# Performance work log

Measured on AMD Instinct MI355X. Metric: run time of the kernel, lower is better.

Reference implementation:

```python
import jax, jax.numpy as jnp
import numpy as np

NUM_HEADS = 8
LN_EPS = 1e-5  # torch.nn.LayerNorm default


def setup_inputs() -> dict:
    key = jax.random.key(0)
    k1, k2, k3, k4 = jax.random.split(key, 4)
    B, S, H = 32, 512, 256
    inputs = jax.random.normal(k1, (B, S, H), dtype=jnp.float32)
    radial_mask = jax.random.uniform(k2, (B, S), dtype=jnp.float32, minval=1e-4, maxval=1.0)
    # torch Linear stores weight as [out, in]; init ~ U(-1/sqrt(in), 1/sqrt(in))
    bound = 1.0 / np.sqrt(H)
    in_proj_w = jax.random.uniform(k3, (3 * H, H), dtype=jnp.float32, minval=-bound, maxval=bound)
    out_proj_w = jax.random.uniform(k4, (H, H), dtype=jnp.float32, minval=-bound, maxval=bound)
    ln_gamma = jnp.ones((H,), dtype=jnp.float32)
    ln_beta = jnp.zeros((H,), dtype=jnp.float32)
    return {
        "inputs": inputs,
        "radial_mask": radial_mask,
        "in_proj_w": in_proj_w,
        "out_proj_w": out_proj_w,
        "ln_gamma": ln_gamma,
        "ln_beta": ln_beta,
    }


def reference(inputs, radial_mask, in_proj_w, out_proj_w, ln_gamma, ln_beta):
    B, S, H = inputs.shape
    nh = NUM_HEADS
    hd = H // nh

    # LayerNorm over the last dim
    mu = jnp.mean(inputs, axis=-1, keepdims=True)
    var = jnp.var(inputs, axis=-1, keepdims=True)
    normed = (inputs - mu) * jax.lax.rsqrt(var + LN_EPS) * ln_gamma + ln_beta

    # QKV projection (no bias); torch Linear: x @ W.T
    qkv = jnp.einsum('bsh,oh->bso', normed, in_proj_w)
    q, k, v = jnp.split(qkv, 3, axis=-1)

    # [B, S, H] -> [B, nh, S, hd]
    def to_heads(x):
        return x.reshape(B, S, nh, hd).transpose(0, 2, 1, 3)

    q = to_heads(q)
    k = to_heads(k)
    v = to_heads(v)

    # Custom transforms before SDPA
    q = q * q + 1e-6
    k = k + jnp.log(radial_mask)[:, None, :, None]

    # scaled_dot_product_attention with default scale = 1/sqrt(hd)
    scale = 1.0 / np.sqrt(hd).astype(np.float32)
    scores = jnp.einsum('bhqd,bhkd->bhqk', q, k) * scale
    attn = jax.nn.softmax(scores, axis=-1)
    out = jnp.einsum('bhqk,bhkd->bhqd', attn, v)

    # back to [B, S, H], output projection, residual with 1/sqrt(2)
    out = out.transpose(0, 2, 1, 3).reshape(B, S, H)
    out = jnp.einsum('bsh,oh->bso', out, out_proj_w)
    return (out + inputs) * np.float32(0.5 ** 0.5)
```

## Files before the change

kernel.cpp:

```cpp
#include <hip/hip_runtime.h>
#include <hip/hip_bf16.h>

typedef unsigned int u32;
typedef unsigned short u16;

#define B_   32
#define S_   512
#define H_   256
#define NH_  8
#define HD_  32

typedef __attribute__((ext_vector_type(8))) short short8;
typedef __attribute__((ext_vector_type(4))) float f32x4;

__device__ __forceinline__ float bfl(u32 u){ union{u32 i;float f;} c; c.i = u << 16;          return c.f; }
__device__ __forceinline__ float bfh(u32 u){ union{u32 i;float f;} c; c.i = u & 0xffff0000u;  return c.f; }
__device__ __forceinline__ float bf1(u16 u){ union{u32 i;float f;} c; c.i = ((u32)u) << 16;   return c.f; }
__device__ __forceinline__ u16   f2b(float f){ __hip_bfloat16 h = __float2bfloat16(f); return *reinterpret_cast<u16*>(&h); }
__device__ __forceinline__ u32   pk2(float a, float b){ return (u32)f2b(a) | ((u32)f2b(b) << 16); }
__device__ __forceinline__ void  unp8(const uint4 u, float* f){
  f[0]=bfl(u.x); f[1]=bfh(u.x); f[2]=bfl(u.y); f[3]=bfh(u.y);
  f[4]=bfl(u.z); f[5]=bfh(u.z); f[6]=bfl(u.w); f[7]=bfh(u.w);
}
__device__ __forceinline__ f32x4 mfma16(short8 a, short8 b, f32x4 c){
  return __builtin_amdgcn_mfma_f32_16x16x32_bf16(a, b, c, 0, 0, 0);
}

template<int F32>
__device__ __forceinline__ void load8(const void* p, int e8, float* f) {
  if (F32) {
    const float4* q = (const float4*)p;
    const float4 a = q[e8 * 2], b = q[e8 * 2 + 1];
    f[0]=a.x; f[1]=a.y; f[2]=a.z; f[3]=a.w; f[4]=b.x; f[5]=b.y; f[6]=b.z; f[7]=b.w;
  } else {
    unp8(((const uint4*)p)[e8], f);
  }
}
template<int F32>
__device__ __forceinline__ void store8(void* p, int e8, const float* f) {
  if (F32) {
    float4* q = (float4*)p;
    q[e8 * 2]     = make_float4(f[0], f[1], f[2], f[3]);
    q[e8 * 2 + 1] = make_float4(f[4], f[5], f[6], f[7]);
  } else {
    uint4 u;
    u.x = pk2(f[0], f[1]); u.y = pk2(f[2], f[3]);
    u.z = pk2(f[4], f[5]); u.w = pk2(f[6], f[7]);
    ((uint4*)p)[e8] = u;
  }
}
template<int F32>
__device__ __forceinline__ float load1(const void* p, size_t e) {
  return F32 ? ((const float*)p)[e] : bf1(((const u16*)p)[e]);
}
template<int F32>
__device__ __forceinline__ short8 loadBfrag(const void* wp, int row, int k0, int K) {
  if (F32) {
    const float* w = (const float*)wp + (size_t)row * K + k0;
    const float4 a = *(const float4*)w;
    const float4 b = *(const float4*)(w + 4);
    short8 r;
    r[0]=(short)f2b(a.x); r[1]=(short)f2b(a.y); r[2]=(short)f2b(a.z); r[3]=(short)f2b(a.w);
    r[4]=(short)f2b(b.x); r[5]=(short)f2b(b.y); r[6]=(short)f2b(b.z); r[7]=(short)f2b(b.w);
    return r;
  } else {
    return *(const short8*)((const u16*)wp + (size_t)row * K + k0);
  }
}

__device__ __forceinline__ int sniff_mode(const void* xin) {
  __shared__ int votes;
  const int tid = threadIdx.x;
  if (tid == 0) votes = 0;
  __syncthreads();
  const u32* xw = (const u32*)xin;
  int h = 0;
#pragma unroll
  for (int j = 0; j < 4; ++j) {
    const u32 u = xw[(tid << 2) + j];
    const u32 e = (u >> 7) & 0xFF;
    h += (e >= 100 && e <= 135) ? 1 : 0;
  }
  if (h) atomicAdd(&votes, h);
  __syncthreads();
  return (votes >= 512) ? 0 : 1;
}

template<int F32>
__global__ __launch_bounds__(256) void ln_qkv_mfma(
    const void* __restrict__ xin, const void* __restrict__ rmask,
    const void* __restrict__ wi, const void* __restrict__ gamma,
    const void* __restrict__ beta,
    u16* __restrict__ qbuf, u16* __restrict__ kbuf, u16* __restrict__ vt)
{
  if (sniff_mode(xin) != F32) return;

  __shared__ __align__(16) u16 XnF[2 * 8 * 64 * 8];
  __shared__ __align__(16) u16 TR[4][32 * 20];
  __shared__ float lmr[32];
  const int tid = threadIdx.x;
  const int l = tid & 63, w = tid >> 6;
  const int lr = l & 15, quad = l >> 4;
  const int row0 = (blockIdx.x >> 1) * 32;
  const int nhalf = blockIdx.x & 1;

  {
    const int r = tid >> 5, ln = tid & 31;
    float g[8], bb[8];
    load8<F32>(gamma, ln, g);
    load8<F32>(beta,  ln, bb);
    const int c = ln >> 2, qd = ln & 3;
#pragma unroll
    for (int p = 0; p < 4; ++p) {
      const int R = p * 8 + r;
      const int grow = row0 + R;
      float x[8]; load8<F32>(xin, grow * 32 + ln, x);
      float s = 0.f, sq = 0.f;
#pragma unroll
      for (int j = 0; j < 8; ++j) { s += x[j]; sq += x[j] * x[j]; }
#pragma unroll
      for (int m = 1; m < 32; m <<= 1) { s += __shfl_xor(s, m); sq += __shfl_xor(sq, m); }
      const float mu  = s * (1.f / 256.f);
      const float var = sq * (1.f / 256.f) - mu * mu;
      const float rs  = rsqrtf(var + 1e-5f);
      short8 pk;
#pragma unroll
      for (int j = 0; j < 8; ++j) pk[j] = (short)f2b((x[j] - mu) * rs * g[j] + bb[j]);
      const int t = R >> 4, rm = R & 15;
      *(short8*)(XnF + (((t * 8 + c) * 64 + qd * 16 + rm) << 3)) = pk;
      if (ln == 0) lmr[R] = logf(load1<F32>(rmask, grow));
    }
  }
  __syncthreads();

  const int bb_ = row0 >> 9;
  const int sB  = (row0 & 511);
  const int tbase = nhalf * 24 + w * 6;
  u16* trw = TR[w];

  short8 BfA[8], BfB[8];
#pragma unroll
  for (int c = 0; c < 8; ++c)
    BfA[c] = loadBfrag<F32>(wi, tbase * 16 + lr, c * 32 + quad * 8, 256);

#pragma unroll
  for (int nt = 0; nt < 6; ++nt) {
    short8* cur = (nt & 1) ? BfB : BfA;
    short8* nxt = (nt & 1) ? BfA : BfB;
    if (nt < 5) {
#pragma unroll
      for (int c = 0; c < 8; ++c)
        nxt[c] = loadBfrag<F32>(wi, (tbase + nt + 1) * 16 + lr, c * 32 + quad * 8, 256);
    }

    f32x4 a0 = {0.f,0.f,0.f,0.f}, a1 = {0.f,0.f,0.f,0.f};
#pragma unroll
    for (int c = 0; c < 8; ++c) {
      const short8 f0 = *(const short8*)(XnF + ((c       * 64 + l) << 3));
      const short8 f1 = *(const short8*)(XnF + (((8 + c) * 64 + l) << 3));
      a0 = mfma16(f0, cur[c], a0);
      a1 = mfma16(f1, cur[c], a1);
    }

    const int nAbs  = (tbase + nt) * 16;
    const int type  = nAbs >> 8;
    const int dbase = nAbs & 255;
    const int bh    = bb_ * NH_ + (dbase >> 5);
    if (type < 2) {
#pragma unroll
      for (int m = 0; m < 2; ++m) {
        const f32x4 acc = m ? a1 : a0;
        const int sL = m * 16 + quad * 4;
#pragma unroll
        for (int i = 0; i < 4; ++i) {
          float v = acc[i];
          v = (type == 0) ? (v * v + 1e-6f) : (v + lmr[sL + i]);
          trw[(sL + i) * 20 + lr] = f2b(v);
        }
      }
      const int s = l >> 1, half = l & 1;
      const uint2 lo = *(const uint2*)(trw + s * 20 + half * 8);
      const uint2 hi = *(const uint2*)(trw + s * 20 + half * 8 + 4);
      uint4 ov; ov.x = lo.x; ov.y = lo.y; ov.z = hi.x; ov.w = hi.y;
      u16* dst = (type == 0) ? qbuf : kbuf;
      *(uint4*)(dst + ((size_t)bh * S_ + sB + s) * HD_ + (dbase & 31) + half * 8) = ov;
    } else {
      const int dd = (dbase & 255) + lr;
#pragma unroll
      for (int m = 0; m < 2; ++m) {
        const f32x4 acc = m ? a1 : a0;
        const int dv = (dbase - 512 + lr) & 255;
        const int hv = dv >> 5, ddv = dv & 31;
        const int bhv = bb_ * NH_ + hv;
        const int slot16 = (((sB >> 5) * 2 + (ddv >> 4)) * 4 + quad) * 16 + (ddv & 15);
        uint2 pkv;
        pkv.x = pk2(acc[0], acc[1]);
        pkv.y = pk2(acc[2], acc[3]);
        *(uint2*)(vt + (size_t)bhv * (S_ * HD_) + slot16 * 8 + m * 4) = pkv;
      }
      (void)dd;
    }
  }
}

__global__ __launch_bounds__(256, 4) void attn_mfma(
    const u16* __restrict__ qbuf, const u16* __restrict__ kbuf,
    const u16* __restrict__ vt, u16* __restrict__ ctx)
{
  __shared__ __align__(16) u16 OB[4][16 * 40];
  const int tid = threadIdx.x;
  const int bh = blockIdx.x & 255, sq = blockIdx.x >> 8;
  const int l = tid & 63, w = tid >> 6;
  const int lr = l & 15, quad = l >> 4;
  const size_t kvbase = (size_t)bh * (S_ * HD_);
  const int q0 = sq * 64 + w * 16;

  const float cE = 0.17677669529663688f * 1.4426950408889634f;

  const short8 qf = *(const short8*)(qbuf + kvbase + (size_t)(q0 + lr) * HD_ + quad * 8);
  const u16* kp = kbuf + kvbase + (size_t)lr * HD_ + quad * 8;
  const u16* vp = vt + kvbase;

  float mS = -1e30f, lS = 0.f;
  f32x4 o0 = {0.f,0.f,0.f,0.f}, o1 = {0.f,0.f,0.f,0.f};

#pragma unroll
  for (int c = 0; c < 4; ++c) {
    f32x4 acc[8];
#pragma unroll
    for (int j = 0; j < 8; ++j) {
      const short8 kf = *(const short8*)(kp + (c * 8 + j) * (16 * HD_));
      f32x4 z = {0.f,0.f,0.f,0.f};
      acc[j] = mfma16(kf, qf, z);
    }

    float mc = acc[0][0];
#pragma unroll
    for (int j = 0; j < 8; ++j)
#pragma unroll
      for (int r = 0; r < 4; ++r) mc = fmaxf(mc, acc[j][r]);
    mc = fmaxf(mc, __shfl_xor(mc, 16));
    mc = fmaxf(mc, __shfl_xor(mc, 32));
    const float mNew  = fmaxf(mS, mc * cE);
    const float alpha = exp2f(mS - mNew);
    float sc = 0.f;
#pragma unroll
    for (int j = 0; j < 8; ++j)
#pragma unroll
      for (int r = 0; r < 4; ++r) {
        const float p = exp2f(fmaf(acc[j][r], cE, -mNew));
        acc[j][r] = p; sc += p;
      }
    sc += __shfl_xor(sc, 16);
    sc += __shfl_xor(sc, 32);
    lS = fmaf(lS, alpha, sc);
    mS = mNew;
#pragma unroll
    for (int r = 0; r < 4; ++r) { o0[r] *= alpha; o1[r] *= alpha; }

#pragma unroll
    for (int g = 0; g < 4; ++g) {
      union { u32 u[4]; short8 s; } pa;
      pa.u[0] = pk2(acc[2*g][0],   acc[2*g][1]);
      pa.u[1] = pk2(acc[2*g][2],   acc[2*g][3]);
      pa.u[2] = pk2(acc[2*g+1][0], acc[2*g+1][1]);
      pa.u[3] = pk2(acc[2*g+1][2], acc[2*g+1][3]);
      const int c16 = c * 4 + g;
      const short8 v0 = *(const short8*)(vp + (((c16 * 8 +     quad) * 16 + lr) << 3));
      const short8 v1 = *(const short8*)(vp + (((c16 * 8 + 4 + quad) * 16 + lr) << 3));
      o0 = mfma16(pa.s, v0, o0);
      o1 = mfma16(pa.s, v1, o1);
    }
  }
  const float inv = 1.f / lS;

  u16* ob = OB[w];
#pragma unroll
  for (int r = 0; r < 4; ++r) {
    const int qq = quad * 4 + r;
    const float iv = __shfl(inv, (l & 48) | qq);
    ob[qq * 40 + lr]      = f2b(o0[r] * iv);
    ob[qq * 40 + 16 + lr] = f2b(o1[r] * iv);
  }
  const uint4 ov = *(const uint4*)(ob + (l >> 2) * 40 + (l & 3) * 8);
  *(uint4*)(ctx + kvbase + (size_t)(q0 + (l >> 2)) * HD_ + (l & 3) * 8) = ov;
}

template<int F32>
__global__ __launch_bounds__(256) void proj_mfma(
    const u16* __restrict__ ctx, const void* __restrict__ xin,
    const void* __restrict__ wo, void* __restrict__ out)
{
  if (sniff_mode(xin) != F32) return;

  __shared__ __align__(16) u16 XnF[8 * 64 * 8];
  __shared__ __align__(16) u16 OutB[16 * 264];
  const int tid = threadIdx.x;
  const int l = tid & 63, w = tid >> 6;
  const int lr = l & 15, quad = l >> 4;
  const int row0 = blockIdx.x * 16;
  const int b = row0 >> 9, s0 = row0 & 511;

#pragma unroll
  for (int it = 0; it < 2; ++it) {
    const int idx = it * 256 + tid;
    const int dq = idx & 3, sl = (idx >> 2) & 15, h = idx >> 6;
    const uint4 cv = *(const uint4*)(ctx + ((size_t)(b * 8 + h) * S_ + s0 + sl) * HD_ + dq * 8);
    const int qds = dq ^ (sl & 3);
    *(uint4*)(XnF + ((h * 64 + qds * 16 + sl) << 3)) = cv;
  }
  __syncthreads();

  const int lsw = (quad ^ (lr & 3)) * 16 + lr;
  short8 BfA[8], BfB[8];
#pragma unroll
  for (int c = 0; c < 8; ++c)
    BfA[c] = loadBfrag<F32>(wo, (w * 4) * 16 + lr, c * 32 + quad * 8, 256);

#pragma unroll
  for (int nt = 0; nt < 4; ++nt) {
    short8* cur = (nt & 1) ? BfB : BfA;
    short8* nxt = (nt & 1) ? BfA : BfB;
    if (nt < 3) {
#pragma unroll
      for (int c = 0; c < 8; ++c)
        nxt[c] = loadBfrag<F32>(wo, (w * 4 + nt + 1) * 16 + lr, c * 32 + quad * 8, 256);
    }
    const int n0 = (w * 4 + nt) * 16;
    f32x4 a0 = {0.f,0.f,0.f,0.f};
#pragma unroll
    for (int c = 0; c < 8; ++c) {
      const short8 f0 = *(const short8*)(XnF + ((c * 64 + lsw) << 3));
      a0 = mfma16(f0, cur[c], a0);
    }
#pragma unroll
    for (int i = 0; i < 4; ++i)
      OutB[(quad * 4 + i) * 264 + n0 + lr] = f2b(a0[i]);
  }
  __syncthreads();

  const int r  = tid >> 4;
  const int c8 = (tid & 15) * 2;
#pragma unroll
  for (int j8 = 0; j8 < 2; ++j8) {
    float xv[8]; load8<F32>(xin, (row0 + r) * 32 + c8 + j8, xv);
    float pv[8]; unp8(*(const uint4*)(OutB + r * 264 + (c8 + j8) * 8), pv);
    float ov[8];
#pragma unroll
    for (int j = 0; j < 8; ++j) ov[j] = (pv[j] + xv[j]) * 0.70710678f;
    store8<F32>(out, (row0 + r) * 32 + c8 + j8, ov);
  }
}

extern "C" void kernel_launch(void* const* d_in, const int* in_sizes, int n_in,
                              void* d_out, int out_size, void* d_ws, size_t ws_size,
                              hipStream_t stream)
{
  const void* xin   = d_in[0];
  const void* rmask = d_in[1];
  const void* wi    = d_in[2];
  const void* wo    = d_in[3];
  const void* gam   = d_in[4];
  const void* bet   = d_in[5];

  u16* q   = (u16*)d_ws;
  u16* k   = q + 4194304;
  u16* vt  = k + 4194304;
  u16* cxb = vt + 4194304;

  ln_qkv_mfma<0><<<1024, 256, 0, stream>>>(xin, rmask, wi, gam, bet, q, k, vt);
  ln_qkv_mfma<1><<<1024, 256, 0, stream>>>(xin, rmask, wi, gam, bet, q, k, vt);
  attn_mfma     <<<2048, 256, 0, stream>>>(q, k, vt, cxb);
  proj_mfma<0>  <<<1024, 256, 0, stream>>>(cxb, xin, wo, d_out);
  proj_mfma<1>  <<<1024, 256, 0, stream>>>(cxb, xin, wo, d_out);
}
```

Before: 204.6 us.

## Enlarge QKV row tile to 64, keep A fragments in registers, direct stores

The LN+QKV kernel now handles 64 rows per block instead of 32, so each weight B-fragment load feeds four MFMA row tiles instead of two. The grid is halved and launch bounds are set to two blocks per CU. The normalized A fragments are hoisted into registers once, and the LDS transpose staging for Q/K is dropped in favour of direct scalar bf16 stores to global. The output projection also hoists its A fragments from LDS, and the dtype-sniff vote now uses a wave ballot instead of per-thread atomics. The trade-off is much higher register pressure and uncoalesced 2-byte Q/K global stores, and the tighter 2-block launch bound may cause spills.

```diff
diff --git a/kernel.cpp b/kernel.cpp
--- a/kernel.cpp
+++ b/kernel.cpp
@@ -81,13 +81,14 @@
     const u32 e = (u >> 7) & 0xFF;
     h += (e >= 100 && e <= 135) ? 1 : 0;
   }
-  if (h) atomicAdd(&votes, h);
-  __syncthreads();
-  return (votes >= 512) ? 0 : 1;
-}
-
-template<int F32>
-__global__ __launch_bounds__(256) void ln_qkv_mfma(
+  const unsigned long long m = __ballot(h >= 3);
+  if ((tid & 63) == 0) atomicAdd(&votes, __popcll(m));
+  __syncthreads();
+  return (votes >= 128) ? 0 : 1;
+}
+
+template<int F32>
+__global__ __launch_bounds__(256, 2) void ln_qkv_mfma(
     const void* __restrict__ xin, const void* __restrict__ rmask,
     const void* __restrict__ wi, const void* __restrict__ gamma,
     const void* __restrict__ beta,
@@ -95,13 +96,12 @@
 {
   if (sniff_mode(xin) != F32) return;
 
-  __shared__ __align__(16) u16 XnF[2 * 8 * 64 * 8];
-  __shared__ __align__(16) u16 TR[4][32 * 20];
-  __shared__ float lmr[32];
+  __shared__ __align__(16) u16 XnF[4 * 8 * 64 * 8];
+  __shared__ float lmr[64];
   const int tid = threadIdx.x;
   const int l = tid & 63, w = tid >> 6;
   const int lr = l & 15, quad = l >> 4;
-  const int row0 = (blockIdx.x >> 1) * 32;
+  const int row0 = (blockIdx.x >> 1) * 64;
   const int nhalf = blockIdx.x & 1;
 
   {
@@ -111,7 +111,7 @@
     load8<F32>(beta,  ln, bb);
     const int c = ln >> 2, qd = ln & 3;
 #pragma unroll
-    for (int p = 0; p < 4; ++p) {
+    for (int p = 0; p < 8; ++p) {
       const int R = p * 8 + r;
       const int grow = row0 + R;
       float x[8]; load8<F32>(xin, grow * 32 + ln, x);
@@ -133,72 +133,72 @@
   }
   __syncthreads();
 
+  short8 Af[4][8];
+#pragma unroll
+  for (int mt = 0; mt < 4; ++mt)
+#pragma unroll
+    for (int c = 0; c < 8; ++c)
+      Af[mt][c] = *(const short8*)(XnF + (((mt * 8 + c) * 64 + l) << 3));
+
   const int bb_ = row0 >> 9;
-  const int sB  = (row0 & 511);
+  const int sB  = row0 & 511;
   const int tbase = nhalf * 24 + w * 6;
-  u16* trw = TR[w];
-
-  short8 BfA[8], BfB[8];
+
+  short8 Bf[2][8];
 #pragma unroll
   for (int c = 0; c < 8; ++c)
-    BfA[c] = loadBfrag<F32>(wi, tbase * 16 + lr, c * 32 + quad * 8, 256);
+    Bf[0][c] = loadBfrag<F32>(wi, tbase * 16 + lr, c * 32 + quad * 8, 256);
 
 #pragma unroll
   for (int nt = 0; nt < 6; ++nt) {
-    short8* cur = (nt & 1) ? BfB : BfA;
-    short8* nxt = (nt & 1) ? BfA : BfB;
+    const int cb = nt & 1;
     if (nt < 5) {
 #pragma unroll
       for (int c = 0; c < 8; ++c)
-        nxt[c] = loadBfrag<F32>(wi, (tbase + nt + 1) * 16 + lr, c * 32 + quad * 8, 256);
-    }
-
-    f32x4 a0 = {0.f,0.f,0.f,0.f}, a1 = {0.f,0.f,0.f,0.f};
+        Bf[cb ^ 1][c] = loadBfrag<F32>(wi, (tbase + nt + 1) * 16 + lr, c * 32 + quad * 8, 256);
+    }
+
+    f32x4 a[4];
+#pragma unroll
+    for (int mt = 0; mt < 4; ++mt) a[mt] = (f32x4){0.f, 0.f, 0.f, 0.f};
 #pragma unroll
     for (int c = 0; c < 8; ++c) {
-      const short8 f0 = *(const short8*)(XnF + ((c       * 64 + l) << 3));
-      const short8 f1 = *(const short8*)(XnF + (((8 + c) * 64 + l) << 3));
-      a0 = mfma16(f0, cur[c], a0);
-      a1 = mfma16(f1, cur[c], a1);
+#pragma unroll
+      for (int mt = 0; mt < 4; ++mt)
+        a[mt] = mfma16(Af[mt][c], Bf[cb][c], a[mt]);
     }
 
     const int nAbs  = (tbase + nt) * 16;
     const int type  = nAbs >> 8;
     const int dbase = nAbs & 255;
-    const int bh    = bb_ * NH_ + (dbase >> 5);
     if (type < 2) {
-#pragma unroll
-      for (int m = 0; m < 2; ++m) {
-        const f32x4 acc = m ? a1 : a0;
-        const int sL = m * 16 + quad * 4;
+      const int d  = dbase + lr;
+      const int h  = d >> 5, dd = d & 31;
+      const int bh = bb_ * NH_ + h;
+      u16* dst = (type == 0) ? qbuf : kbuf;
+#pragma unroll
+      for (int mt = 0; mt < 4; ++mt) {
+        const int sL = mt * 16 + quad * 4;
 #pragma unroll
         for (int i = 0; i < 4; ++i) {
-          float v = acc[i];
+          float v = a[mt][i];
           v = (type == 0) ? (v * v + 1e-6f) : (v + lmr[sL + i]);
-          trw[(sL + i) * 20 + lr] = f2b(v);
+          dst[((size_t)bh * S_ + sB + sL + i) * HD_ + dd] = f2b(v);
         }
       }
-      const int s = l >> 1, half = l & 1;
-      const uint2 lo = *(const uint2*)(trw + s * 20 + half * 8);
-      const uint2 hi = *(const uint2*)(trw + s * 20 + half * 8 + 4);
-      uint4 ov; ov.x = lo.x; ov.y = lo.y; ov.z = hi.x; ov.w = hi.y;
-      u16* dst = (type == 0) ? qbuf : kbuf;
-      *(uint4*)(dst + ((size_t)bh * S_ + sB + s) * HD_ + (dbase & 31) + half * 8) = ov;
     } else {
-      const int dd = (dbase & 255) + lr;
-#pragma unroll
-      for (int m = 0; m < 2; ++m) {
-        const f32x4 acc = m ? a1 : a0;
-        const int dv = (dbase - 512 + lr) & 255;
-        const int hv = dv >> 5, ddv = dv & 31;
-        const int bhv = bb_ * NH_ + hv;
-        const int slot16 = (((sB >> 5) * 2 + (ddv >> 4)) * 4 + quad) * 16 + (ddv & 15);
+      const int dv  = dbase + lr;
+      const int hv  = dv >> 5, ddv = dv & 31;
+      const int bhv = bb_ * NH_ + hv;
+#pragma unroll
+      for (int mt = 0; mt < 4; ++mt) {
+        const int c16 = (sB >> 5) + (mt >> 1);
+        const int slot16 = ((c16 * 2 + (ddv >> 4)) * 4 + quad) * 16 + (ddv & 15);
         uint2 pkv;
-        pkv.x = pk2(acc[0], acc[1]);
-        pkv.y = pk2(acc[2], acc[3]);
-        *(uint2*)(vt + (size_t)bhv * (S_ * HD_) + slot16 * 8 + m * 4) = pkv;
+        pkv.x = pk2(a[mt][0], a[mt][1]);
+        pkv.y = pk2(a[mt][2], a[mt][3]);
+        *(uint2*)(vt + (size_t)bhv * (S_ * HD_) + slot16 * 8 + (mt & 1) * 4) = pkv;
       }
-      (void)dd;
     }
   }
 }
@@ -312,27 +312,29 @@
   __syncthreads();
 
   const int lsw = (quad ^ (lr & 3)) * 16 + lr;
-  short8 BfA[8], BfB[8];
+  short8 Af[8];
 #pragma unroll
   for (int c = 0; c < 8; ++c)
-    BfA[c] = loadBfrag<F32>(wo, (w * 4) * 16 + lr, c * 32 + quad * 8, 256);
+    Af[c] = *(const short8*)(XnF + ((c * 64 + lsw) << 3));
+
+  short8 Bf[2][8];
+#pragma unroll
+  for (int c = 0; c < 8; ++c)
+    Bf[0][c] = loadBfrag<F32>(wo, (w * 4) * 16 + lr, c * 32 + quad * 8, 256);
 
 #pragma unroll
   for (int nt = 0; nt < 4; ++nt) {
-    short8* cur = (nt & 1) ? BfB : BfA;
-    short8* nxt = (nt & 1) ? BfA : BfB;
+    const int cb = nt & 1;
     if (nt < 3) {
 #pragma unroll
       for (int c = 0; c < 8; ++c)
-        nxt[c] = loadBfrag<F32>(wo, (w * 4 + nt + 1) * 16 + lr, c * 32 + quad * 8, 256);
+        Bf[cb ^ 1][c] = loadBfrag<F32>(wo, (w * 4 + nt + 1) * 16 + lr, c * 32 + quad * 8, 256);
     }
     const int n0 = (w * 4 + nt) * 16;
     f32x4 a0 = {0.f,0.f,0.f,0.f};
 #pragma unroll
-    for (int c = 0; c < 8; ++c) {
-      const short8 f0 = *(const short8*)(XnF + ((c * 64 + lsw) << 3));
-      a0 = mfma16(f0, cur[c], a0);
-    }
+    for (int c = 0; c < 8; ++c)
+      a0 = mfma16(Af[c], Bf[cb][c], a0);
 #pragma unroll
     for (int i = 0; i < 4; ++i)
       OutB[(quad * 4 + i) * 264 + n0 + lr] = f2b(a0[i]);
@@ -368,8 +370,8 @@
   u16* vt  = k + 4194304;
   u16* cxb = vt + 4194304;
 
-  ln_qkv_mfma<0><<<1024, 256, 0, stream>>>(xin, rmask, wi, gam, bet, q, k, vt);
-  ln_qkv_mfma<1><<<1024, 256, 0, stream>>>(xin, rmask, wi, gam, bet, q, k, vt);
+  ln_qkv_mfma<0><<<512,  256, 0, stream>>>(xin, rmask, wi, gam, bet, q, k, vt);
+  ln_qkv_mfma<1><<<512,  256, 0, stream>>>(xin, rmask, wi, gam, bet, q, k, vt);
   attn_mfma     <<<2048, 256, 0, stream>>>(q, k, vt, cxb);
   proj_mfma<0>  <<<1024, 256, 0, stream>>>(cxb, xin, wo, d_out);
   proj_mfma<1>  <<<1024, 256, 0, stream>>>(cxb, xin, wo, d_out);
```

Result: faster. 181.0 us (-11.5%).
